# Kernel tuning notes

Measured on AMD Instinct MI355X. Metric: run time of the kernel, lower is better.

## Reference

```python
import jax, jax.numpy as jnp
import numpy as np

N_HEADS = 8
D_K = 256
SCALE = D_K ** -0.5


def setup_inputs() -> dict:
    key = jax.random.key(0)
    k1, k2, k3 = jax.random.split(key, 3)
    B, C, H, W = 8, 256, 32, 32
    x = jax.random.normal(k1, (B, C, H, W), dtype=jnp.float32)
    Wp = jax.random.normal(k2, (C, N_HEADS * D_K * 3), dtype=jnp.float32) * (C ** -0.5)
    bp = jnp.zeros((N_HEADS * D_K * 3,), dtype=jnp.float32)
    Wo = jax.random.normal(k3, (N_HEADS * D_K, C), dtype=jnp.float32) * ((N_HEADS * D_K) ** -0.5)
    bo = jnp.zeros((C,), dtype=jnp.float32)
    return {"x": x, "Wp": Wp, "bp": bp, "Wo": Wo, "bo": bo}


def reference(x, Wp, bp, Wo, bo):
    B, C, H, W = x.shape
    S = H * W
    # [B,C,H,W] -> [B,S,C] tokens
    xt = x.reshape(B, C, S).transpose(0, 2, 1)
    qkv = (xt @ Wp + bp).reshape(B, S, N_HEADS, 3 * D_K)
    q, k, v = jnp.split(qkv, 3, axis=-1)  # each [B,S,H,dk]
    attn = jnp.einsum('bihd,bjhd->bijh', q, k) * SCALE
    attn = jax.nn.softmax(attn, axis=2)  # over j (keys)
    res = jnp.einsum('bijh,bjhd->bihd', attn, v).reshape(B, S, N_HEADS * D_K)
    res = res @ Wo + bo + xt  # residual
    return res.transpose(0, 2, 1).reshape(B, C, H, W)
```

## Files before the change

kernel.cpp:

```cpp
#include <hip/hip_runtime.h>

#define NH    8
#define DK    256
#define SS    1024
#define QSCALE 0.09016844136947155f
#define TSH   8192

using frag8  = __attribute__((ext_vector_type(8))) short;
using f32x16 = __attribute__((ext_vector_type(16))) float;

__device__ __forceinline__ unsigned short f2bf(float f) {
    unsigned int u = __float_as_uint(f);
    return (unsigned short)((u + 0x7FFFu + ((u >> 16) & 1u)) >> 16);
}
__device__ __forceinline__ unsigned int pk2bf(float lo, float hi) {
    unsigned int ul = __float_as_uint(lo), uh = __float_as_uint(hi);
    ul += 0x7FFFu + ((ul >> 16) & 1u);
    uh += 0x7FFFu + ((uh >> 16) & 1u);
    return (ul >> 16) | (uh & 0xFFFF0000u);
}

__device__ __forceinline__ void load_lds16(const void* g, void* l) {
    __builtin_amdgcn_global_load_lds(
        (const __attribute__((address_space(1))) unsigned int*)g,
        (__attribute__((address_space(3))) unsigned int*)l, 16, 0, 0);
}


__global__ __launch_bounds__(256) void k0_all(
    const float* __restrict__ x,  unsigned short* __restrict__ xbT,
    const float* __restrict__ Wp, unsigned short* __restrict__ WptT,
    const float* __restrict__ Wo, unsigned short* __restrict__ WotT)
{
    __shared__ float tile[32][33];
    const int bid = blockIdx.x;
    const float* in; unsigned short* outp; int C, c0, r0; size_t pbase; int psz;
    if (bid < 2048) {
        int rr = bid;
        int b = rr >> 8;
        in = x + (size_t)b * 256 * 1024;
        C = 1024; c0 = (rr & 31) * 32; r0 = ((rr >> 5) & 7) * 32;
        psz = 8192; pbase = (size_t)(b * 32 + (c0 >> 5)); outp = xbT;
    } else if (bid < 3584) {
        int rr = bid - 2048;
        in = Wp; C = 6144; c0 = (rr % 192) * 32; r0 = (rr / 192) * 32;
        psz = 8192; pbase = (size_t)(c0 >> 5); outp = WptT;
    } else {
        int rr = bid - 3584;
        in = Wo; C = 256; c0 = (rr & 7) * 32; r0 = (rr >> 3) * 32;
        psz = 65536; pbase = (size_t)(c0 >> 5); outp = WotT;
    }
    const int tx = threadIdx.x & 31, ty = threadIdx.x >> 5;
#pragma unroll
    for (int j = 0; j < 4; j++)
        tile[ty + j * 8][tx] = in[(size_t)(r0 + ty + j * 8) * C + c0 + tx];
    __syncthreads();
    const int k = r0 + tx;
    unsigned short* dst = outp + pbase * psz + ((k >> 3) * 32) * 8 + (k & 7);
#pragma unroll
    for (int j = 0; j < 4; j++)
        dst[(ty + j * 8) * 8] = f2bf(tile[tx][ty + j * 8]);
}

__global__ __launch_bounds__(256) void k1_qkv(
    const unsigned short* __restrict__ xbT, const unsigned short* __restrict__ WptT,
    const float* __restrict__ bp,
    unsigned short* __restrict__ qb, unsigned short* __restrict__ kb,
    unsigned short* __restrict__ vb)
{
    __shared__ unsigned short Xs[2][4096];
    __shared__ unsigned short Ws[2][4096];
    const int t = threadIdx.x;
    const int wave = t >> 6, lane = t & 63;
    const int l32 = lane & 31, hw = lane >> 5;
    const int n0 = blockIdx.x * 128, m0 = blockIdx.y * 128;
    const int b = m0 >> 10, s0 = m0 & 1023;

    const int h = n0 / 768;
    const int rem = n0 - h * 768;
    const int tt = rem >> 8;
    const int dcol0 = rem & 255;

    const unsigned short* Xg = xbT + (size_t)(b * 32 + (s0 >> 5)) * TSH;
    const unsigned short* Wg = WptT + (size_t)(n0 >> 5) * TSH;

    f32x16 acc[4];
#pragma unroll
    for (int j = 0; j < 4; j++)
#pragma unroll
        for (int r = 0; r < 16; r++) acc[j][r] = 0.f;

    auto stage = [&](int buf, int kt) {
#pragma unroll
        for (int j = 0; j < 4; j++) {
            int rgn = wave * 4 + j;
            if (rgn < 8) {
                int p = rgn >> 1, half = rgn & 1;
                load_lds16(Xg + (size_t)p * TSH + kt * 1024 + half * 512 + lane * 8,
                           &Xs[buf][p * 1024 + half * 512]);
            } else {
                int r2 = rgn - 8, p = r2 >> 1, half = r2 & 1;
                load_lds16(Wg + (size_t)p * TSH + kt * 1024 + half * 512 + lane * 8,
                           &Ws[buf][p * 1024 + half * 512]);
            }
        }
    };

    stage(0, 0);
    __syncthreads();

    for (int kt = 0; kt < 8; kt++) {
        const int cur = kt & 1;
        if (kt < 7) stage(cur ^ 1, kt + 1);
        const unsigned short* Fa = (tt < 2) ? &Ws[cur][wave * 1024] : &Xs[cur][wave * 1024];
        const unsigned short* Fb = (tt < 2) ? &Xs[cur][0] : &Ws[cur][0];
#pragma unroll
        for (int t2 = 0; t2 < 2; t2++) {
            frag8 af = *(const frag8*)(Fa + (2 * t2 + hw) * 256 + l32 * 8);
#pragma unroll
            for (int j = 0; j < 4; j++) {
                frag8 bf = *(const frag8*)(Fb + j * 1024 + (2 * t2 + hw) * 256 + l32 * 8);
                acc[j] = __builtin_amdgcn_mfma_f32_32x32x16_bf16(af, bf, acc[j], 0, 0, 0);
            }
        }
        __syncthreads();
    }

    if (tt < 2) {
        const float sc = (tt == 0) ? QSCALE : 1.0f;
        unsigned short* dst0 = (tt == 0 ? qb : kb);
        const int dc0 = (dcol0 + wave * 32) >> 3;
#pragma unroll
        for (int G = 0; G < 4; G++) {
            float4 bb = *(const float4*)(&bp[n0 + wave * 32 + 4 * hw + 8 * G]);
#pragma unroll
            for (int j = 0; j < 4; j++) {
                unsigned short* cell = dst0
                    + (size_t)((b * NH + h) * 32 + (s0 >> 5) + j) * TSH
                    + ((dc0 + G) * 32 + l32) * 8 + 4 * hw;
                uint2 st;
                st.x = pk2bf((acc[j][4 * G + 0] + bb.x) * sc, (acc[j][4 * G + 1] + bb.y) * sc);
                st.y = pk2bf((acc[j][4 * G + 2] + bb.z) * sc, (acc[j][4 * G + 3] + bb.w) * sc);
                *(uint2*)cell = st;
            }
        }
    } else {
        unsigned short* vt = vb + (size_t)((b * NH + h) * 32 + (s0 >> 5) + wave) * TSH;
#pragma unroll
        for (int j = 0; j < 4; j++) {
            const int d = dcol0 + j * 32 + l32;
            const float bv = bp[n0 + j * 32 + l32];
#pragma unroll
            for (int G = 0; G < 4; G++) {
                int g = G >> 1;
                unsigned short* cell = vt + (g * 2 + hw) * 2048 + d * 8 + 4 * (G & 1);
                uint2 st;
                st.x = pk2bf(acc[j][4 * G + 0] + bv, acc[j][4 * G + 1] + bv);
                st.y = pk2bf(acc[j][4 * G + 2] + bv, acc[j][4 * G + 3] + bv);
                *(uint2*)cell = st;
            }
        }
    }
}

__global__ __launch_bounds__(256, 2) void k2_attn(
    const unsigned short* __restrict__ qb, const unsigned short* __restrict__ kb,
    const unsigned short* __restrict__ vb, unsigned short* __restrict__ ob)
{
    __shared__ unsigned short Ks[2][TSH];
    __shared__ unsigned short Vs[2][TSH];

    const int t = threadIdx.x;
    const int wave = t >> 6, lane = t & 63;
    const int l32 = lane & 31, hw = lane >> 5;

    const int flat = blockIdx.x;
    const int xcd = flat & 7, tt2 = flat >> 3;
    const int qt = tt2 & 7;
    const int bh = xcd * 8 + (tt2 >> 3);

    frag8 qf[16];
    {
        const unsigned short* qp = qb + ((size_t)bh * 32 + qt * 4 + wave) * TSH
                                 + hw * 256 + l32 * 8;
#pragma unroll
        for (int s = 0; s < 16; s++) qf[s] = *(const frag8*)(qp + s * 512);
    }

    f32x16 acc[8];
#pragma unroll
    for (int nb = 0; nb < 8; nb++)
#pragma unroll
        for (int r = 0; r < 16; r++) acc[nb][r] = 0.f;
    float lsum = 0.f;

    const unsigned short* kstg = kb + (size_t)bh * 32 * TSH + wave * 2048 + lane * 8;
    const unsigned short* vstg = vb + (size_t)bh * 32 * TSH + wave * 2048 + lane * 8;

    auto prefetch = [&](int buf, int kt) {
#pragma unroll
        for (int j = 0; j < 4; j++) {
            load_lds16(kstg + (size_t)kt * TSH + j * 512, &Ks[buf][wave * 2048 + j * 512]);
            load_lds16(vstg + (size_t)kt * TSH + j * 512, &Vs[buf][wave * 2048 + j * 512]);
        }
    };

    auto body = [&](const unsigned short* Kb, const unsigned short* Vb) {
        f32x16 sa0, sa1;
#pragma unroll
        for (int r = 0; r < 16; r++) { sa0[r] = 0.f; sa1[r] = 0.f; }
#pragma unroll
        for (int s = 0; s < 16; s += 2) {
            frag8 kf0 = *(const frag8*)(Kb + (2 * s + hw) * 256 + l32 * 8);
            frag8 kf1 = *(const frag8*)(Kb + (2 * s + 2 + hw) * 256 + l32 * 8);
            sa0 = __builtin_amdgcn_mfma_f32_32x32x16_bf16(kf0, qf[s], sa0, 0, 0, 0);
            sa1 = __builtin_amdgcn_mfma_f32_32x32x16_bf16(kf1, qf[s + 1], sa1, 0, 0, 0);
        }
        float p[16];
#pragma unroll
        for (int e = 0; e < 16; e++) {
            p[e] = exp2f(sa0[e] + sa1[e]);
            lsum += p[e];
        }
        frag8 pf[2];
#pragma unroll
        for (int g = 0; g < 2; g++) {
            uint4 w;
            w.x = pk2bf(p[g * 8 + 0], p[g * 8 + 1]);
            w.y = pk2bf(p[g * 8 + 2], p[g * 8 + 3]);
            w.z = pk2bf(p[g * 8 + 4], p[g * 8 + 5]);
            w.w = pk2bf(p[g * 8 + 6], p[g * 8 + 7]);
            pf[g] = *(frag8*)&w;
        }
#pragma unroll
        for (int g = 0; g < 2; g++)
#pragma unroll
            for (int nb = 0; nb < 8; nb++) {
                frag8 vf = *(const frag8*)(Vb + (g * 2 + hw) * 2048 + (nb * 32 + l32) * 8);
                acc[nb] = __builtin_amdgcn_mfma_f32_32x32x16_bf16(vf, pf[g], acc[nb], 0, 0, 0);
            }
    };

    prefetch(0, 0);
    __syncthreads();
    for (int kt = 0; kt < 30; kt += 2) {
        prefetch(1, kt + 1);
        body(&Ks[0][0], &Vs[0][0]);
        __syncthreads();
        prefetch(0, kt + 2);
        body(&Ks[1][0], &Vs[1][0]);
        __syncthreads();
    }
    prefetch(1, 31);
    body(&Ks[0][0], &Vs[0][0]);
    __syncthreads();
    body(&Ks[1][0], &Vs[1][0]);

    lsum += __shfl_xor(lsum, 32);
    const float li = 1.f / lsum;

    unsigned short* opan = ob + ((size_t)bh * 32 + qt * 4 + wave) * TSH;
#pragma unroll
    for (int nb = 0; nb < 8; nb++)
#pragma unroll
        for (int G = 0; G < 4; G++) {
            unsigned short* cell = opan + ((nb * 4 + G) * 32 + l32) * 8 + 4 * hw;
            uint2 st;
            st.x = pk2bf(acc[nb][4 * G + 0] * li, acc[nb][4 * G + 1] * li);
            st.y = pk2bf(acc[nb][4 * G + 2] * li, acc[nb][4 * G + 3] * li);
            *(uint2*)cell = st;
        }
}

__global__ __launch_bounds__(512) void k3_proj(
    const unsigned short* __restrict__ Ob, const unsigned short* __restrict__ WotT,
    const float* __restrict__ bo, const float* __restrict__ x,
    float* __restrict__ out)
{
    __shared__ unsigned short As[2][4096];
    __shared__ unsigned short Bs[2][8192];
    const int t = threadIdx.x;
    const int wave = t >> 6, lane = t & 63;
    const int l32 = lane & 31, hw = lane >> 5;
    const int wc = wave & 1, wt = wave >> 1;
    const int c0 = blockIdx.x * 64, m0 = blockIdx.y * 128;
    const int b = m0 >> 10, s0 = m0 & 1023;

    const unsigned short* Ag = WotT + (size_t)(c0 >> 5) * 65536;

    f32x16 acc;
#pragma unroll
    for (int r = 0; r < 16; r++) acc[r] = 0.f;

    auto stage = [&](int buf, int kt) {
        const int hh = kt >> 2, lc = (kt & 3) * 8;
#pragma unroll
        for (int j = 0; j < 3; j++) {
            int rgn = wave * 3 + j;
            if (rgn < 8) {
                int wp = rgn >> 2, q4 = rgn & 3;
                load_lds16(Ag + (size_t)wp * 65536 + kt * 2048 + q4 * 512 + lane * 8,
                           &As[buf][wp * 2048 + q4 * 512]);
            } else {
                int r2 = rgn - 8, p = r2 >> 2, q4 = r2 & 3;
                load_lds16(Ob + (size_t)((b * NH + hh) * 32 + (s0 >> 5) + p) * TSH
                               + lc * 256 + q4 * 512 + lane * 8,
                           &Bs[buf][p * 2048 + q4 * 512]);
            }
        }
    };

    auto body = [&](const unsigned short* Ab, const unsigned short* Bb) {
#pragma unroll
        for (int t2 = 0; t2 < 4; t2++) {
            frag8 af = *(const frag8*)(Ab + wc * 2048 + (2 * t2 + hw) * 256 + l32 * 8);
            frag8 bf = *(const frag8*)(Bb + wt * 2048 + (2 * t2 + hw) * 256 + l32 * 8);
            acc = __builtin_amdgcn_mfma_f32_32x32x16_bf16(af, bf, acc, 0, 0, 0);
        }
    };

    stage(0, 0);
    __syncthreads();
    for (int kt = 0; kt < 30; kt += 2) {
        stage(1, kt + 1); body(&As[0][0], &Bs[0][0]); __syncthreads();
        stage(0, kt + 2); body(&As[1][0], &Bs[1][0]); __syncthreads();
    }
    stage(1, 31); body(&As[0][0], &Bs[0][0]); __syncthreads();
    body(&As[1][0], &Bs[1][0]);

    const int s = s0 + wt * 32 + l32;
#pragma unroll
    for (int G = 0; G < 4; G++) {
        float4 bb = *(const float4*)(&bo[c0 + wc * 32 + 4 * hw + 8 * G]);
#pragma unroll
        for (int e = 0; e < 4; e++) {
            const int ch = c0 + wc * 32 + 4 * hw + 8 * G + e;
            const float bbe = (e == 0) ? bb.x : (e == 1) ? bb.y : (e == 2) ? bb.z : bb.w;
            size_t off = (size_t)(b * 256 + ch) * 1024 + s;
            out[off] = acc[4 * G + e] + bbe + x[off];
        }
    }
}

extern "C" void kernel_launch(void* const* d_in, const int* in_sizes, int n_in,
                              void* d_out, int out_size, void* d_ws, size_t ws_size,
                              hipStream_t stream)
{
    const float* x  = (const float*)d_in[0];
    const float* Wp = (const float*)d_in[1];
    const float* bp = (const float*)d_in[2];
    const float* Wo = (const float*)d_in[3];
    const float* bo = (const float*)d_in[4];
    float* out = (float*)d_out;

    char* ws = (char*)d_ws;
    unsigned short* qb   = (unsigned short*)(ws);
    unsigned short* kb   = (unsigned short*)(ws + 33554432);
    unsigned short* vb   = (unsigned short*)(ws + 67108864);
    unsigned short* xbT  = (unsigned short*)(ws + 100663296);
    unsigned short* WptT = (unsigned short*)(ws + 104857600);
    unsigned short* WotT = (unsigned short*)(ws + 108003328);

    k0_all<<<dim3(4096), 256, 0, stream>>>(x, xbT, Wp, WptT, Wo, WotT);
    k1_qkv<<<dim3(48, 64), 256, 0, stream>>>(xbT, WptT, bp, qb, kb, vb);
    k2_attn<<<dim3(512), 256, 0, stream>>>(qb, kb, vb, qb );
    k3_proj<<<dim3(4, 64), 512, 0, stream>>>(qb, WotT, bo, x, out);
}
```

Baseline: 221.0 us.

## Load GEMM fragments directly from global memory, dropping LDS staging in QKV and projection

The QKV GEMM and output projection kernels no longer stage tiles into LDS with double buffering and barriers. Each wave now reads its MFMA fragments straight from the pre-swizzled global panels. The projection kernel also moves to 256-thread blocks of 32 output channels, giving twice as many blocks. This removes LDS traffic and __syncthreads stalls, but loses operand sharing across waves and leans on L1/L2 to absorb the repeated global reads.

```diff
diff --git a/kernel.cpp b/kernel.cpp
--- a/kernel.cpp
+++ b/kernel.cpp
@@ -68,8 +68,6 @@
     unsigned short* __restrict__ qb, unsigned short* __restrict__ kb,
     unsigned short* __restrict__ vb)
 {
-    __shared__ unsigned short Xs[2][4096];
-    __shared__ unsigned short Ws[2][4096];
     const int t = threadIdx.x;
     const int wave = t >> 6, lane = t & 63;
     const int l32 = lane & 31, hw = lane >> 5;
@@ -84,46 +82,29 @@
     const unsigned short* Xg = xbT + (size_t)(b * 32 + (s0 >> 5)) * TSH;
     const unsigned short* Wg = WptT + (size_t)(n0 >> 5) * TSH;
 
+    const int fo = hw * 256 + l32 * 8;
+
+    const unsigned short* Ap = (tt < 2) ? (Wg + (size_t)wave * TSH)
+                                        : (Xg + (size_t)wave * TSH);
+    const unsigned short* Bp = (tt < 2) ? Xg : Wg;
+
     f32x16 acc[4];
 #pragma unroll
     for (int j = 0; j < 4; j++)
 #pragma unroll
         for (int r = 0; r < 16; r++) acc[j][r] = 0.f;
 
-    auto stage = [&](int buf, int kt) {
-#pragma unroll
-        for (int j = 0; j < 4; j++) {
-            int rgn = wave * 4 + j;
-            if (rgn < 8) {
-                int p = rgn >> 1, half = rgn & 1;
-                load_lds16(Xg + (size_t)p * TSH + kt * 1024 + half * 512 + lane * 8,
-                           &Xs[buf][p * 1024 + half * 512]);
-            } else {
-                int r2 = rgn - 8, p = r2 >> 1, half = r2 & 1;
-                load_lds16(Wg + (size_t)p * TSH + kt * 1024 + half * 512 + lane * 8,
-                           &Ws[buf][p * 1024 + half * 512]);
-            }
-        }
-    };
-
-    stage(0, 0);
-    __syncthreads();
-
+#pragma unroll
     for (int kt = 0; kt < 8; kt++) {
-        const int cur = kt & 1;
-        if (kt < 7) stage(cur ^ 1, kt + 1);
-        const unsigned short* Fa = (tt < 2) ? &Ws[cur][wave * 1024] : &Xs[cur][wave * 1024];
-        const unsigned short* Fb = (tt < 2) ? &Xs[cur][0] : &Ws[cur][0];
 #pragma unroll
         for (int t2 = 0; t2 < 2; t2++) {
-            frag8 af = *(const frag8*)(Fa + (2 * t2 + hw) * 256 + l32 * 8);
+            frag8 af = *(const frag8*)(Ap + kt * 1024 + t2 * 512 + fo);
 #pragma unroll
             for (int j = 0; j < 4; j++) {
-                frag8 bf = *(const frag8*)(Fb + j * 1024 + (2 * t2 + hw) * 256 + l32 * 8);
+                frag8 bf = *(const frag8*)(Bp + (size_t)j * TSH + kt * 1024 + t2 * 512 + fo);
                 acc[j] = __builtin_amdgcn_mfma_f32_32x32x16_bf16(af, bf, acc[j], 0, 0, 0);
             }
         }
-        __syncthreads();
     }
 
     if (tt < 2) {
@@ -272,69 +253,45 @@
         }
 }
 
-__global__ __launch_bounds__(512) void k3_proj(
+__global__ __launch_bounds__(256) void k3_proj(
     const unsigned short* __restrict__ Ob, const unsigned short* __restrict__ WotT,
     const float* __restrict__ bo, const float* __restrict__ x,
     float* __restrict__ out)
 {
-    __shared__ unsigned short As[2][4096];
-    __shared__ unsigned short Bs[2][8192];
     const int t = threadIdx.x;
     const int wave = t >> 6, lane = t & 63;
     const int l32 = lane & 31, hw = lane >> 5;
-    const int wc = wave & 1, wt = wave >> 1;
-    const int c0 = blockIdx.x * 64, m0 = blockIdx.y * 128;
-    const int b = m0 >> 10, s0 = m0 & 1023;
-
-    const unsigned short* Ag = WotT + (size_t)(c0 >> 5) * 65536;
+    const int c0 = blockIdx.x * 32;
+    const int m = blockIdx.y * 128 + wave * 32;
+    const int b = m >> 10, s0 = m & 1023;
+
+    const unsigned short* Ap = WotT + (size_t)(c0 >> 5) * 65536;
+    const int fo = hw * 256 + l32 * 8;
 
     f32x16 acc;
 #pragma unroll
     for (int r = 0; r < 16; r++) acc[r] = 0.f;
 
-    auto stage = [&](int buf, int kt) {
-        const int hh = kt >> 2, lc = (kt & 3) * 8;
-#pragma unroll
-        for (int j = 0; j < 3; j++) {
-            int rgn = wave * 3 + j;
-            if (rgn < 8) {
-                int wp = rgn >> 2, q4 = rgn & 3;
-                load_lds16(Ag + (size_t)wp * 65536 + kt * 2048 + q4 * 512 + lane * 8,
-                           &As[buf][wp * 2048 + q4 * 512]);
-            } else {
-                int r2 = rgn - 8, p = r2 >> 2, q4 = r2 & 3;
-                load_lds16(Ob + (size_t)((b * NH + hh) * 32 + (s0 >> 5) + p) * TSH
-                               + lc * 256 + q4 * 512 + lane * 8,
-                           &Bs[buf][p * 2048 + q4 * 512]);
-            }
-        }
-    };
-
-    auto body = [&](const unsigned short* Ab, const unsigned short* Bb) {
-#pragma unroll
-        for (int t2 = 0; t2 < 4; t2++) {
-            frag8 af = *(const frag8*)(Ab + wc * 2048 + (2 * t2 + hw) * 256 + l32 * 8);
-            frag8 bf = *(const frag8*)(Bb + wt * 2048 + (2 * t2 + hw) * 256 + l32 * 8);
+#pragma unroll 4
+    for (int kt = 0; kt < 64; kt++) {
+        const int hh = kt >> 3, kc = kt & 7;
+        const unsigned short* Bp = Ob + (size_t)((b * NH + hh) * 32 + (s0 >> 5)) * TSH
+                                 + kc * 1024;
+#pragma unroll
+        for (int t2 = 0; t2 < 2; t2++) {
+            frag8 af = *(const frag8*)(Ap + kt * 1024 + t2 * 512 + fo);
+            frag8 bf = *(const frag8*)(Bp + t2 * 512 + fo);
             acc = __builtin_amdgcn_mfma_f32_32x32x16_bf16(af, bf, acc, 0, 0, 0);
         }
-    };
-
-    stage(0, 0);
-    __syncthreads();
-    for (int kt = 0; kt < 30; kt += 2) {
-        stage(1, kt + 1); body(&As[0][0], &Bs[0][0]); __syncthreads();
-        stage(0, kt + 2); body(&As[1][0], &Bs[1][0]); __syncthreads();
-    }
-    stage(1, 31); body(&As[0][0], &Bs[0][0]); __syncthreads();
-    body(&As[1][0], &Bs[1][0]);
-
-    const int s = s0 + wt * 32 + l32;
+    }
+
+    const int s = s0 + l32;
 #pragma unroll
     for (int G = 0; G < 4; G++) {
-        float4 bb = *(const float4*)(&bo[c0 + wc * 32 + 4 * hw + 8 * G]);
+        float4 bb = *(const float4*)(&bo[c0 + 4 * hw + 8 * G]);
 #pragma unroll
         for (int e = 0; e < 4; e++) {
-            const int ch = c0 + wc * 32 + 4 * hw + 8 * G + e;
+            const int ch = c0 + 4 * hw + 8 * G + e;
             const float bbe = (e == 0) ? bb.x : (e == 1) ? bb.y : (e == 2) ? bb.z : bb.w;
             size_t off = (size_t)(b * 256 + ch) * 1024 + s;
             out[off] = acc[4 * G + e] + bbe + x[off];
@@ -364,5 +321,5 @@
     k0_all<<<dim3(4096), 256, 0, stream>>>(x, xbT, Wp, WptT, Wo, WotT);
     k1_qkv<<<dim3(48, 64), 256, 0, stream>>>(xbT, WptT, bp, qb, kb, vb);
     k2_attn<<<dim3(512), 256, 0, stream>>>(qb, kb, vb, qb );
-    k3_proj<<<dim3(4, 64), 512, 0, stream>>>(qb, WotT, bo, x, out);
-}
+    k3_proj<<<dim3(8, 64), 256, 0, stream>>>(qb, WotT, bo, x, out);
+}
```

New measurement: 263.5 us. +19.2%, slower.
